# Kernel optimization log

Measured on AMD Instinct MI355X. Metric: run time of the kernel, lower is better.

The kernel has to match this reference:

```python
import jax, jax.numpy as jnp
import numpy as np

LATENT_DIM = 32
NB_LABEL = 10
B = 4096


def _conv4(x, w, b):
    # stride-4 kernel-4 conv == non-overlapping 4x4 patch contraction
    Bn, C, H, W = x.shape
    xp = x.reshape(Bn, C, H // 4, 4, W // 4, 4)
    return jnp.einsum('bcipjq,ocpq->boij', xp, w) + b[None, :, None, None]


def _deconv4(x, w, b):
    # stride-4 kernel-4 ConvTranspose2d, padding 0: each pixel expands to a 4x4 block
    Bn, C, H, W = x.shape
    y = jnp.einsum('bcij,copq->boipjq', x, w)  # w: (Cin, Cout, 4, 4)
    return y.reshape(Bn, w.shape[1], H * 4, W * 4) + b[None, :, None, None]


def setup_inputs() -> dict:
    key = jax.random.key(0)
    ks = jax.random.split(key, 24)
    s = 0.05

    def rn(k, shape, scale=s):
        return jax.random.normal(k, shape, dtype=jnp.float32) * scale

    return {
        'x': jax.random.normal(ks[0], (B, 1, 64, 64), dtype=jnp.float32),
        'z': jax.random.normal(ks[1], (B, NB_LABEL), dtype=jnp.float32),
        'u_in': jax.random.normal(ks[2], (B, 2), dtype=jnp.float32),
        'conv1_w': rn(ks[3], (16, 1, 4, 4)), 'conv1_b': rn(ks[4], (16,)),
        'conv2_w': rn(ks[5], (64, 16, 4, 4)), 'conv2_b': rn(ks[6], (64,)),
        'conv3_w': rn(ks[7], (256, 64, 4, 4)), 'conv3_b': rn(ks[8], (256,)),
        'w_xz': rn(ks[9], (32, 256)),
        'w_label': rn(ks[10], (NB_LABEL, 32)),
        'w_zd1': rn(ks[11], (LATENT_DIM, NB_LABEL)),
        'w_zd2': rn(ks[12], (LATENT_DIM, NB_LABEL)),
        'w_xu': rn(ks[13], (32, 256)),
        'w_mu': rn(ks[14], (2, 32)),
        'w_logvar': rn(ks[15], (2, 32)),
        'tc_w': rn(ks[16], (LATENT_DIM, 256, 2)),
        'tc_b': rn(ks[17], (LATENT_DIM, 256)),
        'dec3_w': rn(ks[18], (256, 64, 4, 4)), 'dec3_b': rn(ks[19], (64,)),
        'dec2_w': rn(ks[20], (64, 16, 4, 4)), 'dec2_b': rn(ks[21], (16,)),
        'dec1_w': rn(ks[22], (16, 1, 4, 4)), 'dec1_b': jnp.zeros((1,), dtype=jnp.float32),
    }


def reference(x, z, u_in, conv1_w, conv1_b, conv2_w, conv2_b, conv3_w, conv3_b,
              w_xz, w_label, w_zd1, w_zd2, w_xu, w_mu, w_logvar, tc_w, tc_b,
              dec3_w, dec3_b, dec2_w, dec2_b, dec1_w, dec1_b):
    h = jax.nn.relu(_conv4(x, conv1_w, conv1_b))
    h = jax.nn.relu(_conv4(h, conv2_w, conv2_b))
    h = jax.nn.relu(_conv4(h, conv3_w, conv3_b))
    h = h.reshape(h.shape[0], -1)                       # (B, 256)

    x_z = jax.nn.relu(h @ w_xz.T)                       # (B, 32)
    z_logit = x_z @ w_label.T                           # (B, 10)

    key = jax.random.key(42)
    k_cat, k_eps = jax.random.split(key)
    z_hat = jax.random.categorical(k_cat, z_logit, axis=-1)       # (B,)
    z_onehot = jax.nn.one_hot(z_hat, NB_LABEL, dtype=z_logit.dtype)
    z_d1 = z_onehot @ w_zd1.T                           # (B, 32)
    z_d2 = z_onehot @ w_zd2.T                           # (B, 32)

    x_u = jax.nn.relu(h @ w_xu.T)                       # (B, 32)
    mu = x_u @ w_mu.T                                   # (B, 2)
    logvar = x_u @ w_logvar.T                           # (B, 2)
    std = jnp.exp(0.5 * logvar)
    eps = jax.random.normal(k_eps, std.shape, dtype=std.dtype)
    u_out = eps * std + mu                              # (B, 2)

    # all 32 tiny Linear(2->256)+ReLU collapsed into one batched einsum
    trans = u_out[:, None, :] + jnp.stack([z_d1, z_d2], axis=-1)   # (B, 32, 2)
    x_hat = jax.nn.relu(jnp.einsum('bic,ioc->bio', trans, tc_w) + tc_b[None]).sum(axis=1)  # (B, 256)
    transfo_d1 = trans[:, :, 0]                         # (B, 32)
    transfo_d2 = trans[:, :, 1]

    d = x_hat.reshape(-1, 256, 1, 1)
    d = jax.nn.relu(_deconv4(d, dec3_w, dec3_b))        # (B, 64, 4, 4)
    d = jax.nn.relu(_deconv4(d, dec2_w, dec2_b))        # (B, 16, 16, 16)
    x_hat_logit = _deconv4(d, dec1_w, dec1_b)           # (B, 1, 64, 64)

    return (z_logit, z_hat.reshape(-1, 1), mu, logvar, u_out, x_hat_logit, transfo_d1, transfo_d2)
```

## Files before the change

### kernel.cpp

```cpp
#include <hip/hip_runtime.h>
#include <stdint.h>

#define B_TOT 4096

#define OFF_ZL 0
#define OFF_ZH 40960
#define OFF_MU 45056
#define OFF_LV 53248
#define OFF_UO 61440
#define OFF_XL 69632
#define OFF_T1 16846848
#define OFF_T2 16977920

typedef __attribute__((ext_vector_type(8))) short bf16x8;
typedef __attribute__((ext_vector_type(4))) float f32x4;

__device__ __forceinline__ unsigned short f2b(float f) {
  unsigned int u = __float_as_uint(f);
  return (unsigned short)((u + 0x7FFFu + ((u >> 16) & 1u)) >> 16);
}
__device__ __forceinline__ float b2f(unsigned short b) {
  return __uint_as_float(((unsigned int)b) << 16);
}

#define TF_ROUND(r) do { x0 += x1; x1 = (x1 << (r)) | (x1 >> (32-(r))); x1 ^= x0; } while(0)

__device__ __forceinline__ void threefry(uint32_t k0, uint32_t k1,
                                         uint32_t c0, uint32_t c1,
                                         uint32_t& o0, uint32_t& o1) {
  uint32_t ks2 = k0 ^ k1 ^ 0x1BD11BDAu;
  uint32_t x0 = c0 + k0, x1 = c1 + k1;
  TF_ROUND(13); TF_ROUND(15); TF_ROUND(26); TF_ROUND(6);
  x0 += k1;  x1 += ks2 + 1u;
  TF_ROUND(17); TF_ROUND(29); TF_ROUND(16); TF_ROUND(24);
  x0 += ks2; x1 += k0 + 2u;
  TF_ROUND(13); TF_ROUND(15); TF_ROUND(26); TF_ROUND(6);
  x0 += k0;  x1 += k1 + 3u;
  TF_ROUND(17); TF_ROUND(29); TF_ROUND(16); TF_ROUND(24);
  x0 += k1;  x1 += ks2 + 4u;
  TF_ROUND(13); TF_ROUND(15); TF_ROUND(26); TF_ROUND(6);
  x0 += ks2; x1 += k0 + 5u;
  o0 = x0; o1 = x1;
}

__device__ __forceinline__ uint32_t tf_bits32(uint32_t k0, uint32_t k1, uint32_t j) {
  uint32_t r0, r1;
  threefry(k0, k1, 0u, j, r0, r1);
  return r0 ^ r1;
}

__device__ __forceinline__ float erfinv_xla(float x) {
  float w = -log1pf(-x * x);
  float p;
  if (w < 5.0f) {
    w -= 2.5f;
    p = 2.81022636e-08f;
    p = fmaf(p, w, 3.43273939e-07f);
    p = fmaf(p, w, -3.5233877e-06f);
    p = fmaf(p, w, -4.39150654e-06f);
    p = fmaf(p, w, 0.00021858087f);
    p = fmaf(p, w, -0.00125372503f);
    p = fmaf(p, w, -0.00417768164f);
    p = fmaf(p, w, 0.246640727f);
    p = fmaf(p, w, 1.50140941f);
  } else {
    w = sqrtf(w) - 3.0f;
    p = -0.000200214257f;
    p = fmaf(p, w, 0.000100950558f);
    p = fmaf(p, w, 0.00134934322f);
    p = fmaf(p, w, -0.00367342844f);
    p = fmaf(p, w, 0.00573950773f);
    p = fmaf(p, w, -0.0076224613f);
    p = fmaf(p, w, 0.00943887047f);
    p = fmaf(p, w, 1.00167406f);
    p = fmaf(p, w, 2.83297682f);
  }
  return p * x;
}

__global__ __launch_bounds__(256) void k_prep(const float* __restrict__ w3,
    const float* __restrict__ w2, unsigned short* __restrict__ w3t,
    unsigned short* __restrict__ w2t) {
  int idx = blockIdx.x * 256 + threadIdx.x;
  unsigned short tmp[8];
  if (idx < 32768) {
    int np = idx >> 5, k0 = (idx & 31) * 8;
    int ic = np & 63, pos = np >> 6;
#pragma unroll
    for (int i = 0; i < 8; ++i)
      tmp[i] = f2b(w3[(size_t)(k0 + i) * 1024 + ic * 16 + pos]);
    *(bf16x8*)(w3t + (size_t)np * 256 + k0) = *(bf16x8*)tmp;
  } else if (idx < 32768 + 2048) {
    int j = idx - 32768;
    int n = j >> 3, k0 = (j & 7) * 8;
#pragma unroll
    for (int i = 0; i < 8; ++i)
      tmp[i] = f2b(w2[(size_t)(k0 + i) * 256 + n]);
    *(bf16x8*)(w2t + (size_t)n * 64 + k0) = *(bf16x8*)tmp;
  }
}

__global__ __launch_bounds__(256) void k_conv1(const float* __restrict__ x,
    const float* __restrict__ w, const float* __restrict__ bias,
    float* __restrict__ h1t) {
  __shared__ __align__(16) float ws[256];
  __shared__ float bs[16];
  __shared__ __align__(16) float ds[16 * 264];
  int b = blockIdx.x, t = threadIdx.x;
  ws[t] = w[t];
  if (t < 16) bs[t] = bias[t];
  __syncthreads();
  int i = t >> 4, j = t & 15;
  const float* xb = x + (size_t)b * 4096;
  float4 xv[4];
#pragma unroll
  for (int p = 0; p < 4; ++p)
    xv[p] = *(const float4*)(xb + (4 * i + p) * 64 + 4 * j);
  float acc[16];
#pragma unroll
  for (int oc = 0; oc < 16; ++oc) acc[oc] = bs[oc];
#pragma unroll
  for (int p = 0; p < 4; ++p) {
    float4 xp = xv[p];
#pragma unroll
    for (int oc = 0; oc < 16; ++oc) {
      float4 wv = *(const float4*)(ws + oc * 16 + p * 4);
      acc[oc] = fmaf(xp.x, wv.x, acc[oc]);
      acc[oc] = fmaf(xp.y, wv.y, acc[oc]);
      acc[oc] = fmaf(xp.z, wv.z, acc[oc]);
      acc[oc] = fmaf(xp.w, wv.w, acc[oc]);
    }
  }
  int pos = (i >> 2) * 4 + (j >> 2);
  int pq  = (i & 3) * 4 + (j & 3);
  float* dp = ds + pos * 264 + pq;
#pragma unroll
  for (int oc = 0; oc < 16; ++oc)
    dp[oc * 16] = fmaxf(acc[oc], 0.0f);
  __syncthreads();
  float* hb = h1t + (size_t)b * 4096;
#pragma unroll
  for (int pass = 0; pass < 4; ++pass) {
    int idx = pass * 1024 + t * 4;
    *(float4*)(hb + idx) = *(const float4*)(ds + (idx >> 8) * 264 + (idx & 255));
  }
}

__global__ __launch_bounds__(256) void k_conv2g(const float* __restrict__ A,
    const float* __restrict__ Bw, const float* __restrict__ bias,
    float* __restrict__ h2) {
  __shared__ __align__(16) float As[16][136];
  __shared__ __align__(16) float Bs[16][68];
  int t = threadIdx.x;
  int m0 = blockIdx.x * 128;
  int tx = t & 15, ty = t >> 4;
  float acc[8][4] = {};
  int lrA = t >> 1, lkA = (t & 1) * 8;
  int lrB = t >> 2, lkB = (t & 3) * 4;
  for (int k0 = 0; k0 < 256; k0 += 16) {
    const float* ap = A + (size_t)(m0 + lrA) * 256 + k0 + lkA;
    float4 a0 = *(const float4*)(ap);
    float4 a1 = *(const float4*)(ap + 4);
    float4 bv = *(const float4*)(Bw + (size_t)lrB * 256 + k0 + lkB);
    As[lkA + 0][lrA] = a0.x; As[lkA + 1][lrA] = a0.y;
    As[lkA + 2][lrA] = a0.z; As[lkA + 3][lrA] = a0.w;
    As[lkA + 4][lrA] = a1.x; As[lkA + 5][lrA] = a1.y;
    As[lkA + 6][lrA] = a1.z; As[lkA + 7][lrA] = a1.w;
    Bs[lkB + 0][lrB] = bv.x; Bs[lkB + 1][lrB] = bv.y;
    Bs[lkB + 2][lrB] = bv.z; Bs[lkB + 3][lrB] = bv.w;
    __syncthreads();
#pragma unroll
    for (int kk = 0; kk < 16; ++kk) {
      float4 af0 = *(const float4*)(&As[kk][ty * 8]);
      float4 af1 = *(const float4*)(&As[kk][ty * 8 + 4]);
      float4 bf  = *(const float4*)(&Bs[kk][tx * 4]);
      float av[8] = {af0.x, af0.y, af0.z, af0.w, af1.x, af1.y, af1.z, af1.w};
      float bw[4] = {bf.x, bf.y, bf.z, bf.w};
#pragma unroll
      for (int ii = 0; ii < 8; ++ii)
#pragma unroll
        for (int jj = 0; jj < 4; ++jj)
          acc[ii][jj] = fmaf(av[ii], bw[jj], acc[ii][jj]);
    }
    __syncthreads();
  }
  float4 bb4 = *(const float4*)(bias + tx * 4);
  float bb[4] = {bb4.x, bb4.y, bb4.z, bb4.w};
#pragma unroll
  for (int ii = 0; ii < 8; ++ii) {
    int row = m0 + ty * 8 + ii;
    int b = row >> 4, pos = row & 15;
    float* hp = h2 + (size_t)b * 1024 + pos;
#pragma unroll
    for (int jj = 0; jj < 4; ++jj)
      hp[(tx * 4 + jj) * 16] = fmaxf(acc[ii][jj] + bb[jj], 0.f);
  }
}

__global__ __launch_bounds__(256) void k_conv3p(const float* __restrict__ A,
    const float* __restrict__ w3, float* __restrict__ part) {
  __shared__ __align__(16) float As[16][136];
  __shared__ __align__(16) float Bs[16][68];
  int t = threadIdx.x;
  int m0 = blockIdx.x * 128, n0 = blockIdx.y * 64;
  int kb = blockIdx.z * 256;
  int tx = t & 15, ty = t >> 4;
  float acc[8][4] = {};
  int lrA = t >> 1, lkA = (t & 1) * 8;
  int lrB = t >> 2, lkB = (t & 3) * 4;
  for (int k0 = kb; k0 < kb + 256; k0 += 16) {
    const float* ap = A + (size_t)(m0 + lrA) * 1024 + k0 + lkA;
    float4 a0 = *(const float4*)(ap);
    float4 a1 = *(const float4*)(ap + 4);
    float4 bv = *(const float4*)(w3 + (size_t)(n0 + lrB) * 1024 + k0 + lkB);
    As[lkA + 0][lrA] = a0.x; As[lkA + 1][lrA] = a0.y;
    As[lkA + 2][lrA] = a0.z; As[lkA + 3][lrA] = a0.w;
    As[lkA + 4][lrA] = a1.x; As[lkA + 5][lrA] = a1.y;
    As[lkA + 6][lrA] = a1.z; As[lkA + 7][lrA] = a1.w;
    Bs[lkB + 0][lrB] = bv.x; Bs[lkB + 1][lrB] = bv.y;
    Bs[lkB + 2][lrB] = bv.z; Bs[lkB + 3][lrB] = bv.w;
    __syncthreads();
#pragma unroll
    for (int kk = 0; kk < 16; ++kk) {
      float4 af0 = *(const float4*)(&As[kk][ty * 8]);
      float4 af1 = *(const float4*)(&As[kk][ty * 8 + 4]);
      float4 bf  = *(const float4*)(&Bs[kk][tx * 4]);
      float av[8] = {af0.x, af0.y, af0.z, af0.w, af1.x, af1.y, af1.z, af1.w};
      float bw[4] = {bf.x, bf.y, bf.z, bf.w};
#pragma unroll
      for (int ii = 0; ii < 8; ++ii)
#pragma unroll
        for (int jj = 0; jj < 4; ++jj)
          acc[ii][jj] = fmaf(av[ii], bw[jj], acc[ii][jj]);
    }
    __syncthreads();
  }
  float* pc = part + (size_t)blockIdx.z * 1048576;
#pragma unroll
  for (int ii = 0; ii < 8; ++ii) {
    int row = m0 + ty * 8 + ii;
    *(float4*)(pc + (size_t)row * 256 + n0 + tx * 4) =
        make_float4(acc[ii][0], acc[ii][1], acc[ii][2], acc[ii][3]);
  }
}

__global__ __launch_bounds__(256) void k_headA(const float* __restrict__ part,
    const float* __restrict__ b3,
    const float* __restrict__ w_xz, const float* __restrict__ w_xu,
    float* __restrict__ xzxu) {
  __shared__ __align__(16) float As[16][68];
  __shared__ __align__(16) float Bs[16][68];
  int t = threadIdx.x;
  int m0 = blockIdx.x * 64;
  int tx = t & 15, ty = t >> 4;
  float acc[4][4] = {};
  int lr = t >> 2, lk = (t & 3) * 4;
  const float* wr = (lr < 32) ? (w_xz + lr * 256) : (w_xu + (lr - 32) * 256);
  for (int k0 = 0; k0 < 256; k0 += 16) {
    const float* p0 = part + (size_t)(m0 + lr) * 256 + k0 + lk;
    float4 s  = *(const float4*)(p0);
    float4 s1 = *(const float4*)(p0 + 1048576);
    float4 s2 = *(const float4*)(p0 + 2097152);
    float4 s3 = *(const float4*)(p0 + 3145728);
    float4 bb4 = *(const float4*)(b3 + k0 + lk);
    float4 a;
    a.x = fmaxf(((s.x + s1.x) + s2.x) + s3.x + bb4.x, 0.f);
    a.y = fmaxf(((s.y + s1.y) + s2.y) + s3.y + bb4.y, 0.f);
    a.z = fmaxf(((s.z + s1.z) + s2.z) + s3.z + bb4.z, 0.f);
    a.w = fmaxf(((s.w + s1.w) + s2.w) + s3.w + bb4.w, 0.f);
    float4 bv = *(const float4*)(wr + k0 + lk);
    As[lk + 0][lr] = a.x; As[lk + 1][lr] = a.y; As[lk + 2][lr] = a.z; As[lk + 3][lr] = a.w;
    Bs[lk + 0][lr] = bv.x; Bs[lk + 1][lr] = bv.y; Bs[lk + 2][lr] = bv.z; Bs[lk + 3][lr] = bv.w;
    __syncthreads();
#pragma unroll
    for (int kk = 0; kk < 16; ++kk) {
      float4 af = *(const float4*)(&As[kk][ty * 4]);
      float4 bf = *(const float4*)(&Bs[kk][tx * 4]);
      float av[4] = {af.x, af.y, af.z, af.w};
      float bb[4] = {bf.x, bf.y, bf.z, bf.w};
#pragma unroll
      for (int ii = 0; ii < 4; ++ii)
#pragma unroll
        for (int jj = 0; jj < 4; ++jj)
          acc[ii][jj] = fmaf(av[ii], bb[jj], acc[ii][jj]);
    }
    __syncthreads();
  }
#pragma unroll
  for (int ii = 0; ii < 4; ++ii) {
    int row = m0 + ty * 4 + ii;
    float4 o;
    o.x = fmaxf(acc[ii][0], 0.f);
    o.y = fmaxf(acc[ii][1], 0.f);
    o.z = fmaxf(acc[ii][2], 0.f);
    o.w = fmaxf(acc[ii][3], 0.f);
    *(float4*)(xzxu + (size_t)row * 64 + tx * 4) = o;
  }
}

__global__ __launch_bounds__(256) void k_headB(
    const float* __restrict__ xzxu,
    const float* __restrict__ w_label,
    const float* __restrict__ w_zd1, const float* __restrict__ w_zd2,
    const float* __restrict__ w_mu, const float* __restrict__ w_logvar,
    const float* __restrict__ tc_w, const float* __restrict__ tc_b,
    float* __restrict__ outp, unsigned short* __restrict__ xhb) {
  __shared__ __align__(16) unsigned short twL[16384];
  __shared__ __align__(16) unsigned short tbL[8192];
  __shared__ float xzs[4][32], xus[4][32];
  __shared__ float zls[4][10], gbs[4][10];
  __shared__ float mus[4][2], lvs[4][2], epss[4][2], uos[4][2];
  __shared__ float t1s[4][32], t2s[4][32];
  __shared__ int zhs[4];
  int t = threadIdx.x;
  int wv = t >> 6, l = t & 63;
  int b = blockIdx.x * 4 + wv;

  for (int v = t; v < 4096; v += 256) {
    float4 w4 = *(const float4*)(tc_w + (size_t)v * 4);
    unsigned short pk[4] = {f2b(w4.x), f2b(w4.y), f2b(w4.z), f2b(w4.w)};
    *(ushort4*)(twL + v * 4) = *(ushort4*)pk;
  }
  for (int v = t; v < 2048; v += 256) {
    float4 b4 = *(const float4*)(tc_b + (size_t)v * 4);
    unsigned short pk[4] = {f2b(b4.x), f2b(b4.y), f2b(b4.z), f2b(b4.w)};
    *(ushort4*)(tbL + v * 4) = *(ushort4*)pk;
  }
  {
    float v = xzxu[(size_t)b * 64 + l];
    if (l < 32) xzs[wv][l] = v; else xus[wv][l - 32] = v;
  }
  __syncthreads();

  if (l < 10) {
    float acc = 0.f;
#pragma unroll
    for (int k = 0; k < 32; ++k) acc = fmaf(xzs[wv][k], w_label[l * 32 + k], acc);
    zls[wv][l] = acc;
    outp[OFF_ZL + (size_t)b * 10 + l] = acc;
  } else if (l < 12) {
    int d = l - 10;
    float acc = 0.f;
#pragma unroll
    for (int k = 0; k < 32; ++k) acc = fmaf(xus[wv][k], w_mu[d * 32 + k], acc);
    mus[wv][d] = acc;
    outp[OFF_MU + (size_t)b * 2 + d] = acc;
  } else if (l < 14) {
    int d = l - 12;
    float acc = 0.f;
#pragma unroll
    for (int k = 0; k < 32; ++k) acc = fmaf(xus[wv][k], w_logvar[d * 32 + k], acc);
    lvs[wv][d] = acc;
    outp[OFF_LV + (size_t)b * 2 + d] = acc;
  }
  __syncthreads();

  if (l < 10) {
    uint32_t kc0, kc1;
    threefry(0u, 42u, 0u, 0u, kc0, kc1);
    uint32_t bits = tf_bits32(kc0, kc1, (uint32_t)(b * 10 + l));
    float f = __uint_as_float((bits >> 9) | 0x3F800000u) - 1.0f;
    float u = fmaxf(f, 1.17549435e-38f);
    float g = -logf(-logf(u));
    gbs[wv][l] = zls[wv][l] + g;
  } else if (l < 12) {
    int d = l - 10;
    uint32_t ke0, ke1;
    threefry(0u, 42u, 0u, 1u, ke0, ke1);
    uint32_t bits = tf_bits32(ke0, ke1, (uint32_t)(b * 2 + d));
    float f = __uint_as_float((bits >> 9) | 0x3F800000u) - 1.0f;
    float u = fmaxf(f * 2.0f - 0.99999994f, -0.99999994f);
    epss[wv][d] = 1.41421356f * erfinv_xla(u);
  }
  __syncthreads();

  if (l == 0) {
    float best = gbs[wv][0];
    int bi = 0;
#pragma unroll
    for (int c = 1; c < 10; ++c) {
      float v = gbs[wv][c];
      if (v > best) { best = v; bi = c; }
    }
    zhs[wv] = bi;
    outp[OFF_ZH + b] = (float)bi;
  } else if (l < 3) {
    int d = l - 1;
    float sd = expf(0.5f * lvs[wv][d]);
    float uo = fmaf(epss[wv][d], sd, mus[wv][d]);
    uos[wv][d] = uo;
    outp[OFF_UO + (size_t)b * 2 + d] = uo;
  }
  __syncthreads();

  if (l < 32) {
    int zh = zhs[wv];
    float t1 = uos[wv][0] + w_zd1[l * 10 + zh];
    float t2 = uos[wv][1] + w_zd2[l * 10 + zh];
    t1s[wv][l] = t1; t2s[wv][l] = t2;
    outp[OFF_T1 + (size_t)b * 32 + l] = t1;
    outp[OFF_T2 + (size_t)b * 32 + l] = t2;
  }
  __syncthreads();

  {
    float ax = 0.f, ay = 0.f, az = 0.f, aw = 0.f;
#pragma unroll 4
    for (int i = 0; i < 32; ++i) {
      float t1 = t1s[wv][i], t2 = t2s[wv][i];
      ushort4 wa = *(const ushort4*)(twL + i * 512 + l * 8);
      ushort4 wb = *(const ushort4*)(twL + i * 512 + l * 8 + 4);
      ushort4 tb = *(const ushort4*)(tbL + i * 256 + l * 4);
      float s;
      s = fmaf(t1, b2f(wa.x), fmaf(t2, b2f(wa.y), b2f(tb.x))); ax += fmaxf(s, 0.f);
      s = fmaf(t1, b2f(wa.z), fmaf(t2, b2f(wa.w), b2f(tb.y))); ay += fmaxf(s, 0.f);
      s = fmaf(t1, b2f(wb.x), fmaf(t2, b2f(wb.y), b2f(tb.z))); az += fmaxf(s, 0.f);
      s = fmaf(t1, b2f(wb.z), fmaf(t2, b2f(wb.w), b2f(tb.w))); aw += fmaxf(s, 0.f);
    }
    unsigned short pk[4] = {f2b(ax), f2b(ay), f2b(az), f2b(aw)};
    *(ushort4*)(xhb + (size_t)b * 256 + l * 4) = *(ushort4*)pk;
  }
}

__global__ __launch_bounds__(256) void k_dec3m(const unsigned short* __restrict__ xhb,
    const unsigned short* __restrict__ w3t, const float* __restrict__ bias,
    unsigned short* __restrict__ d3t) {
  int t = threadIdx.x;
  int lane = t & 63, wv = t >> 6;
  int m0 = blockIdx.x * 64, n0 = blockIdx.y * 64;
  int l15 = lane & 15, g8 = (lane >> 4) * 8;
  const unsigned short* arow = xhb + (size_t)(m0 + wv * 16 + l15) * 256 + g8;
  const unsigned short* brow = w3t + (size_t)(n0 + l15) * 256 + g8;
  f32x4 acc[4] = {};
  for (int kb = 0; kb < 256; kb += 32) {
    bf16x8 af = *(const bf16x8*)(arow + kb);
#pragma unroll
    for (int ns = 0; ns < 4; ++ns) {
      bf16x8 bf = *(const bf16x8*)(brow + (size_t)ns * 4096 + kb);
      acc[ns] = __builtin_amdgcn_mfma_f32_16x16x32_bf16(af, bf, acc[ns], 0, 0, 0);
    }
  }
  int rbase = (lane >> 4) * 4;
#pragma unroll
  for (int ns = 0; ns < 4; ++ns) {
    int ncol = n0 + ns * 16 + l15;
    float bb = bias[ncol & 63];
#pragma unroll
    for (int r = 0; r < 4; ++r) {
      float v = fmaxf(acc[ns][r] + bb, 0.f);
      d3t[(size_t)(m0 + wv * 16 + rbase + r) * 1024 + ncol] = f2b(v);
    }
  }
}

__global__ __launch_bounds__(256) void k_dec2m(const unsigned short* __restrict__ d3t,
    const unsigned short* __restrict__ w2t, const float* __restrict__ b2,
    const float* __restrict__ w1, const float* __restrict__ b1,
    float* __restrict__ outp) {
  __shared__ unsigned short d2L[4][4096];
  __shared__ __align__(16) float w1s[256];
  __shared__ float b1s;
  int t = threadIdx.x;
  int lane = t & 63, wv = t >> 6;
  int m0 = blockIdx.x * 64;
  w1s[t] = w1[t];
  if (t == 0) b1s = b1[0];
  int l15 = lane & 15, g8 = (lane >> 4) * 8;
  const unsigned short* arow = d3t + (size_t)(m0 + wv * 16 + l15) * 64 + g8;
  bf16x8 af0 = *(const bf16x8*)(arow);
  bf16x8 af1 = *(const bf16x8*)(arow + 32);
  const unsigned short* brow = w2t + (size_t)l15 * 64 + g8;
  f32x4 acc[16] = {};
#pragma unroll
  for (int ns = 0; ns < 16; ++ns) {
    bf16x8 bf0 = *(const bf16x8*)(brow + (size_t)ns * 1024);
    bf16x8 bf1 = *(const bf16x8*)(brow + (size_t)ns * 1024 + 32);
    acc[ns] = __builtin_amdgcn_mfma_f32_16x16x32_bf16(af0, bf0, acc[ns], 0, 0, 0);
    acc[ns] = __builtin_amdgcn_mfma_f32_16x16x32_bf16(af1, bf1, acc[ns], 0, 0, 0);
  }
  int rbase = (lane >> 4) * 4;
  int pq_p = l15 >> 2, pq_q = l15 & 3;
#pragma unroll
  for (int ns = 0; ns < 16; ++ns) {
    float bb = b2[ns];
#pragma unroll
    for (int r = 0; r < 4; ++r) {
      int pos = rbase + r;
      float v = fmaxf(acc[ns][r] + bb, 0.f);
      d2L[wv][ns * 256 + ((pos >> 2) * 4 + pq_p) * 16 + (pos & 3) * 4 + pq_q] = f2b(v);
    }
  }
  __syncthreads();
  int bg0 = m0 >> 4;
  for (int c4 = 0; c4 < 16; ++c4) {
    int v = t + 256 * c4;
    int bp = v >> 10;
    int I = (v & 1023) >> 4;
    int jpix = v & 15;
    int ipix = I >> 2, pp = I & 3;
    const unsigned short* dl = &d2L[bp][ipix * 16 + jpix];
    float4 o = make_float4(b1s, b1s, b1s, b1s);
#pragma unroll
    for (int c = 0; c < 16; ++c) {
      float dv = b2f(dl[c * 256]);
      float4 wv4 = *(const float4*)(w1s + c * 16 + pp * 4);
      o.x = fmaf(dv, wv4.x, o.x);
      o.y = fmaf(dv, wv4.y, o.y);
      o.z = fmaf(dv, wv4.z, o.z);
      o.w = fmaf(dv, wv4.w, o.w);
    }
    *(float4*)(outp + (size_t)(bg0 + bp) * 4096 + I * 64 + jpix * 4) = o;
  }
}

extern "C" void kernel_launch(void* const* d_in, const int* in_sizes, int n_in,
                              void* d_out, int out_size, void* d_ws, size_t ws_size,
                              hipStream_t stream) {
  const float* x       = (const float*)d_in[0];
  const float* conv1_w = (const float*)d_in[3];
  const float* conv1_b = (const float*)d_in[4];
  const float* conv2_w = (const float*)d_in[5];
  const float* conv2_b = (const float*)d_in[6];
  const float* conv3_w = (const float*)d_in[7];
  const float* conv3_b = (const float*)d_in[8];
  const float* w_xz    = (const float*)d_in[9];
  const float* w_label = (const float*)d_in[10];
  const float* w_zd1   = (const float*)d_in[11];
  const float* w_zd2   = (const float*)d_in[12];
  const float* w_xu    = (const float*)d_in[13];
  const float* w_mu    = (const float*)d_in[14];
  const float* w_logvar= (const float*)d_in[15];
  const float* tc_w    = (const float*)d_in[16];
  const float* tc_b    = (const float*)d_in[17];
  const float* dec3_w  = (const float*)d_in[18];
  const float* dec3_b  = (const float*)d_in[19];
  const float* dec2_w  = (const float*)d_in[20];
  const float* dec2_b  = (const float*)d_in[21];
  const float* dec1_w  = (const float*)d_in[22];
  const float* dec1_b  = (const float*)d_in[23];

  float* out = (float*)d_out;
  float* ws  = (float*)d_ws;

  float* big = out + OFF_XL;
  float* h2  = ws;
  unsigned short* d3t = (unsigned short*)ws;
  unsigned short* xhb = (unsigned short*)(ws + 5242880);
  unsigned short* w3t = (unsigned short*)(ws + 5767168);
  unsigned short* w2t = (unsigned short*)(ws + 5898240);
  float* xzxu = ws + 5906432;

  k_prep<<<136, 256, 0, stream>>>(dec3_w, dec2_w, w3t, w2t);
  k_conv1<<<B_TOT, 256, 0, stream>>>(x, conv1_w, conv1_b, big);
  k_conv2g<<<512, 256, 0, stream>>>(big, conv2_w, conv2_b, h2);
  k_conv3p<<<dim3(32, 4, 4), 256, 0, stream>>>(h2, conv3_w, big);
  k_headA<<<64, 256, 0, stream>>>(big, conv3_b, w_xz, w_xu, xzxu);
  k_headB<<<B_TOT / 4, 256, 0, stream>>>(xzxu, w_label, w_zd1, w_zd2, w_mu,
                                         w_logvar, tc_w, tc_b, out, xhb);
  k_dec3m<<<dim3(64, 16), 256, 0, stream>>>(xhb, w3t, dec3_b, d3t);
  k_dec2m<<<1024, 256, 0, stream>>>(d3t, w2t, dec2_b, dec1_w, dec1_b, big);
}
```

Before: 188.0 us.

## Fuse conv1 and conv2 into one kernel keeping conv1 output in LDS

Merges the conv1 kernel and the conv2 GEMM kernel so that each block computes conv1 for 4 images directly into shared memory and then runs the conv2 GEMM from there. This removes the 64 MB round trip of the conv1 activation through global memory and one kernel launch. In exchange each block recomputes over smaller M tiles (64 rows), uses larger LDS (about 40 KB) and splits K into two halves with extra syncs, which may lower occupancy and GEMM efficiency.

```diff
diff --git a/kernel.cpp b/kernel.cpp
--- a/kernel.cpp
+++ b/kernel.cpp
@@ -100,97 +100,83 @@
   }
 }
 
-__global__ __launch_bounds__(256) void k_conv1(const float* __restrict__ x,
-    const float* __restrict__ w, const float* __restrict__ bias,
-    float* __restrict__ h1t) {
-  __shared__ __align__(16) float ws[256];
-  __shared__ float bs[16];
-  __shared__ __align__(16) float ds[16 * 264];
-  int b = blockIdx.x, t = threadIdx.x;
-  ws[t] = w[t];
-  if (t < 16) bs[t] = bias[t];
+__global__ __launch_bounds__(256, 3) void k_conv12(const float* __restrict__ x,
+    const float* __restrict__ w1c, const float* __restrict__ b1c,
+    const float* __restrict__ w2, const float* __restrict__ b2c,
+    float* __restrict__ h2) {
+  __shared__ __align__(16) float As[128][68];
+  __shared__ __align__(16) float Bs[16][68];
+  __shared__ __align__(16) float w1s[256];
+  __shared__ float b1v[16];
+  int t = threadIdx.x, blk = blockIdx.x;
+  w1s[t] = w1c[t];
+  if (t < 16) b1v[t] = b1c[t];
   __syncthreads();
   int i = t >> 4, j = t & 15;
-  const float* xb = x + (size_t)b * 4096;
-  float4 xv[4];
-#pragma unroll
-  for (int p = 0; p < 4; ++p)
-    xv[p] = *(const float4*)(xb + (4 * i + p) * 64 + 4 * j);
-  float acc[16];
-#pragma unroll
-  for (int oc = 0; oc < 16; ++oc) acc[oc] = bs[oc];
-#pragma unroll
-  for (int p = 0; p < 4; ++p) {
-    float4 xp = xv[p];
-#pragma unroll
-    for (int oc = 0; oc < 16; ++oc) {
-      float4 wv = *(const float4*)(ws + oc * 16 + p * 4);
-      acc[oc] = fmaf(xp.x, wv.x, acc[oc]);
-      acc[oc] = fmaf(xp.y, wv.y, acc[oc]);
-      acc[oc] = fmaf(xp.z, wv.z, acc[oc]);
-      acc[oc] = fmaf(xp.w, wv.w, acc[oc]);
-    }
-  }
-  int pos = (i >> 2) * 4 + (j >> 2);
-  int pq  = (i & 3) * 4 + (j & 3);
-  float* dp = ds + pos * 264 + pq;
-#pragma unroll
-  for (int oc = 0; oc < 16; ++oc)
-    dp[oc * 16] = fmaxf(acc[oc], 0.0f);
-  __syncthreads();
-  float* hb = h1t + (size_t)b * 4096;
-#pragma unroll
-  for (int pass = 0; pass < 4; ++pass) {
-    int idx = pass * 1024 + t * 4;
-    *(float4*)(hb + idx) = *(const float4*)(ds + (idx >> 8) * 264 + (idx & 255));
-  }
-}
-
-__global__ __launch_bounds__(256) void k_conv2g(const float* __restrict__ A,
-    const float* __restrict__ Bw, const float* __restrict__ bias,
-    float* __restrict__ h2) {
-  __shared__ __align__(16) float As[16][136];
-  __shared__ __align__(16) float Bs[16][68];
-  int t = threadIdx.x;
-  int m0 = blockIdx.x * 128;
+  int pos = ((i >> 2) << 2) + (j >> 2);
+  int pq  = ((i & 3) << 2) + (j & 3);
   int tx = t & 15, ty = t >> 4;
-  float acc[8][4] = {};
-  int lrA = t >> 1, lkA = (t & 1) * 8;
   int lrB = t >> 2, lkB = (t & 3) * 4;
-  for (int k0 = 0; k0 < 256; k0 += 16) {
-    const float* ap = A + (size_t)(m0 + lrA) * 256 + k0 + lkA;
-    float4 a0 = *(const float4*)(ap);
-    float4 a1 = *(const float4*)(ap + 4);
-    float4 bv = *(const float4*)(Bw + (size_t)lrB * 256 + k0 + lkB);
-    As[lkA + 0][lrA] = a0.x; As[lkA + 1][lrA] = a0.y;
-    As[lkA + 2][lrA] = a0.z; As[lkA + 3][lrA] = a0.w;
-    As[lkA + 4][lrA] = a1.x; As[lkA + 5][lrA] = a1.y;
-    As[lkA + 6][lrA] = a1.z; As[lkA + 7][lrA] = a1.w;
-    Bs[lkB + 0][lrB] = bv.x; Bs[lkB + 1][lrB] = bv.y;
-    Bs[lkB + 2][lrB] = bv.z; Bs[lkB + 3][lrB] = bv.w;
+  float acc[4][4] = {};
+  const float* xbase = x + (size_t)blk * 4 * 4096;
+
+#pragma unroll 1
+  for (int half = 0; half < 2; ++half) {
+#pragma unroll 1
+    for (int bb = 0; bb < 4; ++bb) {
+      const float* xb = xbase + bb * 4096;
+      float4 xv0 = *(const float4*)(xb + (4 * i + 0) * 64 + 4 * j);
+      float4 xv1 = *(const float4*)(xb + (4 * i + 1) * 64 + 4 * j);
+      float4 xv2 = *(const float4*)(xb + (4 * i + 2) * 64 + 4 * j);
+      float4 xv3 = *(const float4*)(xb + (4 * i + 3) * 64 + 4 * j);
+      int row = bb * 16 + pos;
+      float a1[8];
+#pragma unroll
+      for (int o = 0; o < 8; ++o) a1[o] = b1v[half * 8 + o];
+#pragma unroll
+      for (int o = 0; o < 8; ++o) {
+        const float* wv = w1s + (half * 8 + o) * 16;
+        float a = a1[o];
+        a = fmaf(xv0.x, wv[0],  a); a = fmaf(xv0.y, wv[1],  a);
+        a = fmaf(xv0.z, wv[2],  a); a = fmaf(xv0.w, wv[3],  a);
+        a = fmaf(xv1.x, wv[4],  a); a = fmaf(xv1.y, wv[5],  a);
+        a = fmaf(xv1.z, wv[6],  a); a = fmaf(xv1.w, wv[7],  a);
+        a = fmaf(xv2.x, wv[8],  a); a = fmaf(xv2.y, wv[9],  a);
+        a = fmaf(xv2.z, wv[10], a); a = fmaf(xv2.w, wv[11], a);
+        a = fmaf(xv3.x, wv[12], a); a = fmaf(xv3.y, wv[13], a);
+        a = fmaf(xv3.z, wv[14], a); a = fmaf(xv3.w, wv[15], a);
+        As[o * 16 + pq][row] = fmaxf(a, 0.f);
+      }
+    }
     __syncthreads();
-#pragma unroll
-    for (int kk = 0; kk < 16; ++kk) {
-      float4 af0 = *(const float4*)(&As[kk][ty * 8]);
-      float4 af1 = *(const float4*)(&As[kk][ty * 8 + 4]);
-      float4 bf  = *(const float4*)(&Bs[kk][tx * 4]);
-      float av[8] = {af0.x, af0.y, af0.z, af0.w, af1.x, af1.y, af1.z, af1.w};
-      float bw[4] = {bf.x, bf.y, bf.z, bf.w};
-#pragma unroll
-      for (int ii = 0; ii < 8; ++ii)
-#pragma unroll
-        for (int jj = 0; jj < 4; ++jj)
-          acc[ii][jj] = fmaf(av[ii], bw[jj], acc[ii][jj]);
-    }
-    __syncthreads();
-  }
-  float4 bb4 = *(const float4*)(bias + tx * 4);
+#pragma unroll 1
+    for (int k0 = 0; k0 < 128; k0 += 16) {
+      float4 bv = *(const float4*)(w2 + (size_t)lrB * 256 + half * 128 + k0 + lkB);
+      Bs[lkB + 0][lrB] = bv.x; Bs[lkB + 1][lrB] = bv.y;
+      Bs[lkB + 2][lrB] = bv.z; Bs[lkB + 3][lrB] = bv.w;
+      __syncthreads();
+#pragma unroll
+      for (int kk = 0; kk < 16; ++kk) {
+        float4 af = *(const float4*)(&As[k0 + kk][ty * 4]);
+        float4 bf = *(const float4*)(&Bs[kk][tx * 4]);
+        float av[4] = {af.x, af.y, af.z, af.w};
+        float bw[4] = {bf.x, bf.y, bf.z, bf.w};
+#pragma unroll
+        for (int ii = 0; ii < 4; ++ii)
+#pragma unroll
+          for (int jj = 0; jj < 4; ++jj)
+            acc[ii][jj] = fmaf(av[ii], bw[jj], acc[ii][jj]);
+      }
+      __syncthreads();
+    }
+  }
+  float4 bb4 = *(const float4*)(b2c + tx * 4);
   float bb[4] = {bb4.x, bb4.y, bb4.z, bb4.w};
 #pragma unroll
-  for (int ii = 0; ii < 8; ++ii) {
-    int row = m0 + ty * 8 + ii;
-    int b = row >> 4, pos = row & 15;
-    float* hp = h2 + (size_t)b * 1024 + pos;
+  for (int ii = 0; ii < 4; ++ii) {
+    int row = blk * 64 + ty * 4 + ii;
+    int b = row >> 4, pos2 = row & 15;
+    float* hp = h2 + (size_t)b * 1024 + pos2;
 #pragma unroll
     for (int jj = 0; jj < 4; ++jj)
       hp[(tx * 4 + jj) * 16] = fmaxf(acc[ii][jj] + bb[jj], 0.f);
@@ -551,8 +537,7 @@
   float* xzxu = ws + 5906432;
 
   k_prep<<<136, 256, 0, stream>>>(dec3_w, dec2_w, w3t, w2t);
-  k_conv1<<<B_TOT, 256, 0, stream>>>(x, conv1_w, conv1_b, big);
-  k_conv2g<<<512, 256, 0, stream>>>(big, conv2_w, conv2_b, h2);
+  k_conv12<<<1024, 256, 0, stream>>>(x, conv1_w, conv1_b, conv2_w, conv2_b, h2);
   k_conv3p<<<dim3(32, 4, 4), 256, 0, stream>>>(h2, conv3_w, big);
   k_headA<<<64, 256, 0, stream>>>(big, conv3_b, w_xz, w_xu, xzxu);
   k_headB<<<B_TOT / 4, 256, 0, stream>>>(xzxu, w_label, w_zd1, w_zd2, w_mu,
```

Result: slower. 414.8 us (+120.6%).
